# Kernel optimization log

Hardware: AMD Instinct MI355X
Metric: run time of the kernel (lower is better)

The kernel has to match this reference:

```python
import jax, jax.numpy as jnp
import numpy as np

INPDIM = 512
RECDIM = 512


def setup_inputs() -> dict:
    key = jax.random.key(0)
    k1, k2, k3, k4 = jax.random.split(key, 4)
    x = jax.random.normal(k1, (64, 1024, INPDIM), dtype=jnp.float32)
    W = jax.random.normal(k2, (INPDIM, RECDIM), dtype=jnp.float32) / np.sqrt(INPDIM)
    # per-unit recurrent weight vector, kept in (-1, 1) for stability
    u = jax.random.uniform(k3, (RECDIM,), dtype=jnp.float32, minval=-1.0, maxval=1.0)
    b = jax.random.normal(k4, (RECDIM,), dtype=jnp.float32) * 0.01
    return {"x": x, "W": W, "u": u, "b": b}


def reference(x, W, u, b):
    # IndRNN: h_t = relu(x_t @ W + u * h_{t-1} + b), h_0 = ones(recdim)
    B, T, _ = x.shape
    # Batch the input projection as one big GEMM (time-independent part).
    xp = jnp.einsum('bti,ir->btr', x, W) + b  # [B, T, R]
    h0 = jnp.ones((B, W.shape[1]), dtype=x.dtype)

    def step(h, xp_t):
        h = jax.nn.relu(xp_t + u * h)
        return h, h

    _, hs = jax.lax.scan(step, h0, jnp.swapaxes(xp, 0, 1))  # hs: [T, B, R]
    return jnp.swapaxes(hs, 0, 1)  # [B, T, R]
```

## Files before the change

kernel.cpp:

```cpp
#include <hip/hip_runtime.h>
#include <hip/hip_fp16.h>
#include <hip/hip_bf16.h>
#include <stdint.h>

#define TILE 128
#define BK 32
#define LDST 40

typedef __attribute__((ext_vector_type(8))) short short8;
typedef __attribute__((ext_vector_type(8))) unsigned short ushort8;
typedef __attribute__((ext_vector_type(4))) float f32x4;

static __device__ __forceinline__ unsigned short f2bf(float f) {
    union { float f; uint32_t u; } v; v.f = f;
    uint32_t u = v.u;
    u += 0x7fffu + ((u >> 16) & 1u);
    return (unsigned short)(u >> 16);
}

static __device__ __forceinline__ unsigned int pk_bf16(float a, float b) {
    __hip_bfloat162 h = __float22bfloat162_rn(float2{a, b});
    union { __hip_bfloat162 h; unsigned int u; } c; c.h = h;
    return c.u;
}

__global__ __launch_bounds__(256)
void wt_kernel(const float* __restrict__ W, unsigned short* __restrict__ Wt)
{
    __shared__ float s[32][33];
    const int tx = threadIdx.x;
    const int ty = threadIdx.y;
    const int kBase = blockIdx.x * 32;
    const int nBase = blockIdx.y * 32;
    #pragma unroll
    for (int j = 0; j < 4; ++j)
        s[ty + 8 * j][tx] = W[(size_t)(kBase + ty + 8 * j) * 512 + nBase + tx];
    __syncthreads();
    #pragma unroll
    for (int j = 0; j < 4; ++j)
        Wt[(size_t)(nBase + ty + 8 * j) * 512 + kBase + tx] = f2bf(s[tx][ty + 8 * j]);
}

template <bool F16OUT>
__global__ __launch_bounds__(256, 4)
void gemm_bias_kernel(const float* __restrict__ X, const unsigned short* __restrict__ Wt,
                      const float* __restrict__ bias,
                      float* __restrict__ out32, __half* __restrict__ xpT)
{
    __shared__ unsigned short As[TILE * LDST];
    __shared__ unsigned short Bs[TILE * LDST];

    const int tid = threadIdx.x;

    const int lin = blockIdx.x;
    const int xcd = lin & 7;
    const int idx = lin >> 3;
    const int rowBase = (xcd * 64 + (idx >> 2)) * TILE;
    const int colBase = (idx & 3) * TILE;

    const int wave  = tid >> 6;
    const int lane  = tid & 63;
    const int m16   = lane & 15;
    const int quad  = lane >> 4;
    const int waveM = wave & 1;
    const int waveN = wave >> 1;

    f32x4 acc[4][4] = {};

    const int srow = tid >> 2;
    const int sc4  = tid & 3;

    for (int kt = 0; kt < 512; kt += BK) {
        #pragma unroll
        for (int p = 0; p < 2; ++p) {
            int r = p * 64 + srow;
            const float* src = X + (size_t)(rowBase + r) * 512 + kt + sc4 * 8;
            float4 v0 = *(const float4*)(src);
            float4 v1 = *(const float4*)(src + 4);
            union { ushort8 s8; unsigned int u[4]; } us;
            us.u[0] = pk_bf16(v0.x, v0.y); us.u[1] = pk_bf16(v0.z, v0.w);
            us.u[2] = pk_bf16(v1.x, v1.y); us.u[3] = pk_bf16(v1.z, v1.w);
            *(ushort8*)(&As[r * LDST + sc4 * 8]) = us.s8;
        }
        #pragma unroll
        for (int p = 0; p < 2; ++p) {
            int n = p * 64 + srow;
            ushort8 v = *(const ushort8*)(Wt + (size_t)(colBase + n) * 512 + kt + sc4 * 8);
            *(ushort8*)(&Bs[n * LDST + sc4 * 8]) = v;
        }
        __syncthreads();

        short8 a_frag[4], b_frag[4];
        #pragma unroll
        for (int mi = 0; mi < 4; ++mi)
            a_frag[mi] = *(const short8*)&As[(waveM * 64 + mi * 16 + m16) * LDST + quad * 8];
        #pragma unroll
        for (int ni = 0; ni < 4; ++ni)
            b_frag[ni] = *(const short8*)&Bs[(waveN * 64 + ni * 16 + m16) * LDST + quad * 8];

        #pragma unroll
        for (int mi = 0; mi < 4; ++mi)
            #pragma unroll
            for (int ni = 0; ni < 4; ++ni) {
                if (F16OUT)
                    acc[mi][ni] = __builtin_amdgcn_mfma_f32_16x16x32_bf16(
                        b_frag[ni], a_frag[mi], acc[mi][ni], 0, 0, 0);
                else
                    acc[mi][ni] = __builtin_amdgcn_mfma_f32_16x16x32_bf16(
                        a_frag[mi], b_frag[ni], acc[mi][ni], 0, 0, 0);
            }
        __syncthreads();
    }

    if (F16OUT) {
        const int bb = rowBase >> 10;
        #pragma unroll
        for (int ni = 0; ni < 4; ++ni) {
            int r0 = colBase + waveN * 64 + ni * 16 + quad * 4;
            float4 b4 = *(const float4*)&bias[r0];
            #pragma unroll
            for (int mi = 0; mi < 4; ++mi) {
                int tt = (rowBase + waveM * 64 + mi * 16 + m16) & 1023;
                #pragma unroll
                for (int r = 0; r < 4; ++r) {
                    float v = acc[mi][ni][r] + ((const float*)&b4)[r];
                    xpT[((size_t)bb * 512 + r0 + r) * 1024 + tt] = __float2half_rn(v);
                }
            }
        }
    } else {
        #pragma unroll
        for (int ni = 0; ni < 4; ++ni) {
            int col = colBase + waveN * 64 + ni * 16 + m16;
            float bv = bias[col];
            #pragma unroll
            for (int mi = 0; mi < 4; ++mi) {
                int row0 = rowBase + waveM * 64 + mi * 16 + quad * 4;
                #pragma unroll
                for (int r = 0; r < 4; ++r) {
                    float v = acc[mi][ni][r] + bv;
                    out32[(size_t)(row0 + r) * 512 + col] = v;
                }
            }
        }
    }
}

#define SUNR 128

__global__ __launch_bounds__(64)
void scan_t_kernel(const __half* __restrict__ xpT, float* __restrict__ out,
                   const float* __restrict__ u)
{
    const int gid = blockIdx.x * 64 + threadIdx.x;
    const int b = gid >> 9;
    const int r = gid & 511;
    const float ur = u[r];
    const unsigned short* p = (const unsigned short*)xpT + ((size_t)b * 512 + r) * 1024;
    float* po = out + (size_t)b * 1024 * 512 + r;

    float h = 1.0f;
    ushort8 cur[SUNR / 8], nxt[SUNR / 8];
    #pragma unroll
    for (int j = 0; j < SUNR / 8; ++j) cur[j] = *(const ushort8*)(p + j * 8);

    for (int t0 = 0; t0 < 1024; t0 += SUNR) {
        const bool more = (t0 + SUNR) < 1024;
        if (more) {
            #pragma unroll
            for (int j = 0; j < SUNR / 8; ++j)
                nxt[j] = *(const ushort8*)(p + t0 + SUNR + j * 8);
        }
        #pragma unroll
        for (int j = 0; j < SUNR / 8; ++j) {
            #pragma unroll
            for (int e = 0; e < 8; ++e) {
                float xv = __half2float(__ushort_as_half(cur[j][e]));
                h = fmaxf(fmaf(ur, h, xv), 0.0f);
                __builtin_nontemporal_store(h, po + (size_t)(t0 + j * 8 + e) * 512);
            }
        }
        #pragma unroll
        for (int j = 0; j < SUNR / 8; ++j) cur[j] = nxt[j];
    }
}

#define UNR 32
__global__ __launch_bounds__(64)
void scan_f32_kernel(float* __restrict__ out, const float* __restrict__ u)
{
    const int gid = blockIdx.x * 64 + threadIdx.x;
    const int b = gid >> 9;
    const int r = gid & 511;
    const float ur = u[r];
    float* p = out + (size_t)b * 1024 * 512 + r;

    float h = 1.0f;
    float cur[UNR], nxt[UNR];
    #pragma unroll
    for (int j = 0; j < UNR; ++j) cur[j] = p[(size_t)j * 512];

    for (int t0 = 0; t0 < 1024; t0 += UNR) {
        const bool more = (t0 + UNR) < 1024;
        const float* pn = p + (size_t)(t0 + UNR) * 512;
        if (more) {
            #pragma unroll
            for (int j = 0; j < UNR; ++j) nxt[j] = pn[(size_t)j * 512];
        }
        #pragma unroll
        for (int j = 0; j < UNR; ++j) {
            h = fmaxf(fmaf(ur, h, cur[j]), 0.0f);
            p[(size_t)(t0 + j) * 512] = h;
        }
        #pragma unroll
        for (int j = 0; j < UNR; ++j) cur[j] = nxt[j];
    }
}

extern "C" void kernel_launch(void* const* d_in, const int* in_sizes, int n_in,
                              void* d_out, int out_size, void* d_ws, size_t ws_size,
                              hipStream_t stream) {
    const float* x = (const float*)d_in[0];
    const float* W = (const float*)d_in[1];
    const float* u = (const float*)d_in[2];
    const float* b = (const float*)d_in[3];
    float* out = (float*)d_out;

    const size_t WT_BYTES = (size_t)512 * 512 * 2;
    const size_t XP_BYTES = (size_t)64 * 1024 * 512 * 2;
    unsigned short* Wt = (unsigned short*)d_ws;
    __half* xp16 = (__half*)((char*)d_ws + WT_BYTES);
    const bool f16path = ws_size >= WT_BYTES + XP_BYTES;

    dim3 tgrid(16, 16), tblk(32, 8);
    wt_kernel<<<tgrid, tblk, 0, stream>>>(W, Wt);

    dim3 grid(2048);
    if (f16path) {
        gemm_bias_kernel<true><<<grid, 256, 0, stream>>>(x, Wt, b, nullptr, xp16);
        scan_t_kernel<<<512, 64, 0, stream>>>(xp16, out, u);
    } else {
        gemm_bias_kernel<false><<<grid, 256, 0, stream>>>(x, Wt, b, out, nullptr);
        scan_f32_kernel<<<512, 64, 0, stream>>>(out, u);
    }
}
```

Baseline: 292.1 us.

## Pre-convert X to bf16 and stage GEMM tiles with direct global-to-LDS loads

Adds a separate pass that converts the fp32 input to bf16 once, writing into the output buffer as scratch. The GEMM then loads A and B tiles with global_load_lds straight into unpadded shared memory, removing the per-tile fp32-to-bf16 conversion and register staging. Occupancy hints change from 4 to 2 blocks. In exchange there is an extra full read and write of X (64M elements), and the unpadded LDS layout may add bank conflicts on fragment reads.

```diff
diff --git a/kernel.cpp b/kernel.cpp
--- a/kernel.cpp
+++ b/kernel.cpp
@@ -10,6 +10,9 @@
 typedef __attribute__((ext_vector_type(8))) short short8;
 typedef __attribute__((ext_vector_type(8))) unsigned short ushort8;
 typedef __attribute__((ext_vector_type(4))) float f32x4;
+
+typedef const __attribute__((address_space(1))) void* gptr_t;
+typedef __attribute__((address_space(3))) void* lptr_t;
 
 static __device__ __forceinline__ unsigned short f2bf(float f) {
     union { float f; uint32_t u; } v; v.f = f;
@@ -41,17 +44,114 @@
         Wt[(size_t)(nBase + ty + 8 * j) * 512 + kBase + tx] = f2bf(s[tx][ty + 8 * j]);
 }
 
-template <bool F16OUT>
-__global__ __launch_bounds__(256, 4)
-void gemm_bias_kernel(const float* __restrict__ X, const unsigned short* __restrict__ Wt,
-                      const float* __restrict__ bias,
-                      float* __restrict__ out32, __half* __restrict__ xpT)
+__global__ __launch_bounds__(256)
+void xb_kernel(const float* __restrict__ X, unsigned short* __restrict__ Xb)
+{
+    size_t i = ((size_t)blockIdx.x * 256 + threadIdx.x) * 16;
+    const size_t stride = (size_t)2048 * 256 * 16;
+    #pragma unroll
+    for (int it = 0; it < 4; ++it, i += stride) {
+        float4 v0 = *(const float4*)(X + i);
+        float4 v1 = *(const float4*)(X + i + 4);
+        float4 v2 = *(const float4*)(X + i + 8);
+        float4 v3 = *(const float4*)(X + i + 12);
+        union { ushort8 s8; unsigned int u[4]; } a, b;
+        a.u[0] = pk_bf16(v0.x, v0.y); a.u[1] = pk_bf16(v0.z, v0.w);
+        a.u[2] = pk_bf16(v1.x, v1.y); a.u[3] = pk_bf16(v1.z, v1.w);
+        b.u[0] = pk_bf16(v2.x, v2.y); b.u[1] = pk_bf16(v2.z, v2.w);
+        b.u[2] = pk_bf16(v3.x, v3.y); b.u[3] = pk_bf16(v3.z, v3.w);
+        *(ushort8*)(Xb + i)     = a.s8;
+        *(ushort8*)(Xb + i + 8) = b.s8;
+    }
+}
+
+__global__ __launch_bounds__(256, 2)
+void gemm_xb_kernel(const unsigned short* __restrict__ Xb, const unsigned short* __restrict__ Wt,
+                    const float* __restrict__ bias, __half* __restrict__ xpT)
+{
+    __shared__ unsigned short As[TILE * BK];
+    __shared__ unsigned short Bs[TILE * BK];
+
+    const int tid = threadIdx.x;
+
+    const int lin = blockIdx.x;
+    const int xcd = lin & 7;
+    const int idx = lin >> 3;
+    const int rowBase = (xcd * 64 + (idx >> 2)) * TILE;
+    const int colBase = (idx & 3) * TILE;
+
+    const int wave  = tid >> 6;
+    const int lane  = tid & 63;
+    const int m16   = lane & 15;
+    const int quad  = lane >> 4;
+    const int waveM = wave & 1;
+    const int waveN = wave >> 1;
+
+    f32x4 acc[4][4] = {};
+
+    const int c0 = wave * 2 * 64 + lane;
+    const int m0 = c0 >> 2, j0 = c0 & 3;
+    const int c1 = (wave * 2 + 1) * 64 + lane;
+    const int m1 = c1 >> 2, j1 = c1 & 3;
+
+    const unsigned short* aS0 = Xb + (size_t)(rowBase + m0) * 512 + j0 * 8;
+    const unsigned short* aS1 = Xb + (size_t)(rowBase + m1) * 512 + j1 * 8;
+    const unsigned short* bS0 = Wt + (size_t)(colBase + m0) * 512 + j0 * 8;
+    const unsigned short* bS1 = Wt + (size_t)(colBase + m1) * 512 + j1 * 8;
+
+    for (int kt = 0; kt < 512; kt += BK) {
+        __builtin_amdgcn_global_load_lds((gptr_t)(aS0 + kt),
+            (lptr_t)((char*)As + (wave * 2) * 64 * 16), 16, 0, 0);
+        __builtin_amdgcn_global_load_lds((gptr_t)(aS1 + kt),
+            (lptr_t)((char*)As + (wave * 2 + 1) * 64 * 16), 16, 0, 0);
+        __builtin_amdgcn_global_load_lds((gptr_t)(bS0 + kt),
+            (lptr_t)((char*)Bs + (wave * 2) * 64 * 16), 16, 0, 0);
+        __builtin_amdgcn_global_load_lds((gptr_t)(bS1 + kt),
+            (lptr_t)((char*)Bs + (wave * 2 + 1) * 64 * 16), 16, 0, 0);
+        __syncthreads();
+
+        short8 a_frag[4], b_frag[4];
+        #pragma unroll
+        for (int mi = 0; mi < 4; ++mi)
+            a_frag[mi] = *(const short8*)&As[(waveM * 64 + mi * 16 + m16) * BK + quad * 8];
+        #pragma unroll
+        for (int ni = 0; ni < 4; ++ni)
+            b_frag[ni] = *(const short8*)&Bs[(waveN * 64 + ni * 16 + m16) * BK + quad * 8];
+
+        #pragma unroll
+        for (int mi = 0; mi < 4; ++mi)
+            #pragma unroll
+            for (int ni = 0; ni < 4; ++ni)
+                acc[mi][ni] = __builtin_amdgcn_mfma_f32_16x16x32_bf16(
+                    b_frag[ni], a_frag[mi], acc[mi][ni], 0, 0, 0);
+        __syncthreads();
+    }
+
+    const int bb = rowBase >> 10;
+    #pragma unroll
+    for (int ni = 0; ni < 4; ++ni) {
+        int r0 = colBase + waveN * 64 + ni * 16 + quad * 4;
+        float4 b4 = *(const float4*)&bias[r0];
+        #pragma unroll
+        for (int mi = 0; mi < 4; ++mi) {
+            int tt = (rowBase + waveM * 64 + mi * 16 + m16) & 1023;
+            #pragma unroll
+            for (int r = 0; r < 4; ++r) {
+                float v = acc[mi][ni][r] + ((const float*)&b4)[r];
+                xpT[((size_t)bb * 512 + r0 + r) * 1024 + tt] = __float2half_rn(v);
+            }
+        }
+    }
+}
+
+__global__ __launch_bounds__(256, 2)
+void gemm_f32_kernel(const float* __restrict__ X, const unsigned short* __restrict__ Wt,
+                     const float* __restrict__ bias, float* __restrict__ out32)
 {
     __shared__ unsigned short As[TILE * LDST];
     __shared__ unsigned short Bs[TILE * LDST];
 
     const int tid = threadIdx.x;
-
     const int lin = blockIdx.x;
     const int xcd = lin & 7;
     const int idx = lin >> 3;
@@ -101,46 +201,23 @@
         #pragma unroll
         for (int mi = 0; mi < 4; ++mi)
             #pragma unroll
-            for (int ni = 0; ni < 4; ++ni) {
-                if (F16OUT)
-                    acc[mi][ni] = __builtin_amdgcn_mfma_f32_16x16x32_bf16(
-                        b_frag[ni], a_frag[mi], acc[mi][ni], 0, 0, 0);
-                else
-                    acc[mi][ni] = __builtin_amdgcn_mfma_f32_16x16x32_bf16(
-                        a_frag[mi], b_frag[ni], acc[mi][ni], 0, 0, 0);
-            }
+            for (int ni = 0; ni < 4; ++ni)
+                acc[mi][ni] = __builtin_amdgcn_mfma_f32_16x16x32_bf16(
+                    a_frag[mi], b_frag[ni], acc[mi][ni], 0, 0, 0);
         __syncthreads();
     }
 
-    if (F16OUT) {
-        const int bb = rowBase >> 10;
-        #pragma unroll
-        for (int ni = 0; ni < 4; ++ni) {
-            int r0 = colBase + waveN * 64 + ni * 16 + quad * 4;
-            float4 b4 = *(const float4*)&bias[r0];
-            #pragma unroll
-            for (int mi = 0; mi < 4; ++mi) {
-                int tt = (rowBase + waveM * 64 + mi * 16 + m16) & 1023;
-                #pragma unroll
-                for (int r = 0; r < 4; ++r) {
-                    float v = acc[mi][ni][r] + ((const float*)&b4)[r];
-                    xpT[((size_t)bb * 512 + r0 + r) * 1024 + tt] = __float2half_rn(v);
-                }
-            }
-        }
-    } else {
-        #pragma unroll
-        for (int ni = 0; ni < 4; ++ni) {
-            int col = colBase + waveN * 64 + ni * 16 + m16;
-            float bv = bias[col];
-            #pragma unroll
-            for (int mi = 0; mi < 4; ++mi) {
-                int row0 = rowBase + waveM * 64 + mi * 16 + quad * 4;
-                #pragma unroll
-                for (int r = 0; r < 4; ++r) {
-                    float v = acc[mi][ni][r] + bv;
-                    out32[(size_t)(row0 + r) * 512 + col] = v;
-                }
+    #pragma unroll
+    for (int ni = 0; ni < 4; ++ni) {
+        int col = colBase + waveN * 64 + ni * 16 + m16;
+        float bv = bias[col];
+        #pragma unroll
+        for (int mi = 0; mi < 4; ++mi) {
+            int row0 = rowBase + waveM * 64 + mi * 16 + quad * 4;
+            #pragma unroll
+            for (int r = 0; r < 4; ++r) {
+                float v = acc[mi][ni][r] + bv;
+                out32[(size_t)(row0 + r) * 512 + col] = v;
             }
         }
     }
@@ -235,12 +312,13 @@
     dim3 tgrid(16, 16), tblk(32, 8);
     wt_kernel<<<tgrid, tblk, 0, stream>>>(W, Wt);
 
-    dim3 grid(2048);
     if (f16path) {
-        gemm_bias_kernel<true><<<grid, 256, 0, stream>>>(x, Wt, b, nullptr, xp16);
+        unsigned short* Xb = (unsigned short*)out;
+        xb_kernel<<<2048, 256, 0, stream>>>(x, Xb);
+        gemm_xb_kernel<<<2048, 256, 0, stream>>>(Xb, Wt, b, xp16);
         scan_t_kernel<<<512, 64, 0, stream>>>(xp16, out, u);
     } else {
-        gemm_bias_kernel<false><<<grid, 256, 0, stream>>>(x, Wt, b, out, nullptr);
+        gemm_f32_kernel<<<2048, 256, 0, stream>>>(x, Wt, b, out);
         scan_f32_kernel<<<512, 64, 0, stream>>>(out, u);
     }
 }
```

Result: no change. 291.7 us (-0.1%).
